# Kernel optimization log

Measured on AMD Instinct MI355X. Metric: run time of the kernel, lower is better.

Reference implementation:

```python
import jax, jax.numpy as jnp
import numpy as np

N = 100000
E = 3200000
CH_IN = 128
HID = 128
CH_OUT = 3


def setup_inputs() -> dict:
    key = jax.random.key(0)
    ks = jax.random.split(key, 16)
    def lin(kw, fan_in, fan_out):
        bound = 1.0 / np.sqrt(fan_in)
        kw1, kw2 = jax.random.split(kw)
        W = jax.random.uniform(kw1, (fan_in, fan_out), jnp.float32, -bound, bound)
        b = jax.random.uniform(kw2, (fan_out,), jnp.float32, -bound, bound)
        return W, b
    x = jax.random.normal(ks[0], (N, CH_IN), jnp.float32)
    edge_index = jax.random.randint(ks[1], (2, E), 0, N, jnp.int64)
    W1, b1 = lin(ks[2], CH_IN, HID)
    W2, b2 = lin(ks[3], HID, HID)
    lw1, lb1 = lin(ks[4], HID, HID)
    lw2, lb2 = lin(ks[5], HID, HID)
    lw3, lb3 = lin(ks[6], HID, HID)
    lw4, lb4 = lin(ks[7], HID, CH_OUT)
    return {"x": x, "edge_index": edge_index,
            "W1": W1, "b1": b1, "W2": W2, "b2": b2,
            "lw1": lw1, "lb1": lb1, "lw2": lw2, "lb2": lb2,
            "lw3": lw3, "lb3": lb3, "lw4": lw4, "lb4": lb4}


def gcn_conv(x, W, b, src, dst, n_nodes):
    xw = x @ W  # [N, H]
    ew = jnp.ones(src.shape[0], x.dtype)
    deg = jax.ops.segment_sum(ew, dst, num_segments=n_nodes) + 2.0  # +2 from improved self-loop
    dinv = jnp.where(deg > 0, jax.lax.rsqrt(deg), 0.0)
    norm = dinv[src] * dinv[dst]  # [E]
    agg = jax.ops.segment_sum(xw[src] * norm[:, None], dst, num_segments=n_nodes)
    # self-loop contribution: weight 2 * dinv[i]^2 * xw[i]
    agg = agg + xw * (2.0 * dinv * dinv)[:, None]
    return agg + b


def reference(x, edge_index, W1, b1, W2, b2, lw1, lb1, lw2, lb2, lw3, lb3, lw4, lb4):
    src, dst = edge_index[0], edge_index[1]
    n = x.shape[0]
    h = jnp.tanh(gcn_conv(x, W1, b1, src, dst, n))
    h = jnp.tanh(gcn_conv(h, W2, b2, src, dst, n))
    # dropout in eval mode = identity
    h = jnp.tanh(h @ lw1 + lb1)
    h = jnp.tanh(h @ lw2 + lb2)
    h = jnp.tanh(h @ lw3 + lb3)
    return h @ lw4 + lb4
```

## Files before the change

### kernel.cpp

```cpp
#include <hip/hip_runtime.h>

typedef __attribute__((ext_vector_type(8))) short short8;
typedef __attribute__((ext_vector_type(4))) float floatx4;
typedef __attribute__((ext_vector_type(4))) unsigned int uintx4;
typedef unsigned int uint32;

__device__ inline float b2f(unsigned short u) {
    union { uint32 i; float f; } x; x.i = ((uint32)u) << 16; return x.f;
}
__device__ inline float bl(uint32 v) {
    union { uint32 i; float f; } x; x.i = v << 16; return x.f;
}
__device__ inline float bh(uint32 v) {
    union { uint32 i; float f; } x; x.i = v & 0xffff0000u; return x.f;
}
__device__ inline unsigned short f2b(float f) {
    union { float f; uint32 u; } x; x.f = f;
    uint32 r = x.u + 0x7fffu + ((x.u >> 16) & 1u);
    return (unsigned short)(r >> 16);
}
__device__ inline float fast_tanh(float x) {
    float ax = __builtin_fabsf(x);
    float t = __builtin_amdgcn_exp2f(-2.8853900817779268f * ax);
    float r = (1.0f - t) * __builtin_amdgcn_rcpf(1.0f + t);
    return __builtin_copysignf(r, x);
}


#define CHUNK 8192
#define MAXBK 512
#define CAP   8704
#define LSTR  136

__global__ __launch_bounds__(512, 2) void scatterb_k(const int* __restrict__ eidx,
                                                     uint32* __restrict__ bkt_cur,
                                                     uint32* __restrict__ packed, int E,
                                                     const float* __restrict__ w0,
                                                     const float* __restrict__ w1,
                                                     const float* __restrict__ w2,
                                                     const float* __restrict__ w3,
                                                     const float* __restrict__ w4,
                                                     unsigned short* __restrict__ Wt_hi,
                                                     unsigned short* __restrict__ Wt_lo) {
    __shared__ uint32 hist[MAXBK];
    __shared__ uint32 hsc[MAXBK];
    __shared__ uint32 gbase[MAXBK];
    __shared__ uint32 lcur[MAXBK];
    __shared__ uint32 wsum[8];
    __shared__ uint32 stage[CHUNK];
    __shared__ unsigned short stgb[CHUNK];
    int t = threadIdx.x;

    if (blockIdx.x < 20) {
        int u = blockIdx.x * 512 + t;
        int widx = u >> 11;
        int f8 = u & 2047;
        const float* W;
        switch (widx) {
            case 0: W = w0; break;
            case 1: W = w1; break;
            case 2: W = w2; break;
            case 3: W = w3; break;
            default: W = w4; break;
        }
        int ct = f8 >> 8, kc = (f8 >> 6) & 3, quad = (f8 >> 4) & 3, r = f8 & 15;
        int c = ct * 16 + r;
        int kbase = kc * 32 + quad * 8;
        short8 hi8, lo8;
#pragma unroll
        for (int j = 0; j < 8; ++j) {
            float w = W[(kbase + j) * 128 + c];
            unsigned short h = f2b(w);
            hi8[j] = (short)h;
            lo8[j] = (short)f2b(w - b2f(h));
        }
        *(short8*)(Wt_hi + widx * 16384 + f8 * 8) = hi8;
        *(short8*)(Wt_lo + widx * 16384 + f8 * 8) = lo8;
    }

    int cbase = blockIdx.x * CHUNK;
    int n = E - cbase; if (n > CHUNK) n = CHUNK;

    hist[t] = 0;
    __syncthreads();
    int dreg[CHUNK / 512];
    int nt = 0;
    for (int i = t; i < n; i += 512) {
        int d = eidx[E + cbase + i];
        dreg[nt++] = d;
        atomicAdd(&hist[d >> 8], 1u);
    }
    __syncthreads();
    uint32 v = hist[t];
    uint32 x = v;
    int lane = t & 63;
#pragma unroll
    for (int off = 1; off < 64; off <<= 1) {
        uint32 y = __shfl_up(x, off);
        if (lane >= off) x += y;
    }
    if (lane == 63) wsum[t >> 6] = x;
    __syncthreads();
    uint32 pre = 0;
#pragma unroll
    for (int w = 0; w < 8; ++w) pre += (w < (t >> 6)) ? wsum[w] : 0;
    uint32 excl = x + pre - v;
    hsc[t] = excl;
    lcur[t] = excl;
    if (v) gbase[t] = (uint32)t * CAP + atomicAdd(&bkt_cur[t], v);
    __syncthreads();
    nt = 0;
    for (int i = t; i < n; i += 512) {
        int s = eidx[cbase + i];
        int d = dreg[nt++];
        int b = d >> 8;
        uint32 pos = atomicAdd(&lcur[b], 1u);
        stage[pos] = ((uint32)s << 8) | (uint32)(d & 255);
        stgb[pos] = (unsigned short)b;
    }
    __syncthreads();
    for (int i = t; i < n; i += 512) {
        int b = stgb[i];
        packed[gbase[b] + (i - hsc[b])] = stage[i];
    }
}


__global__ __launch_bounds__(256) void buildb_gemm_k(
    const uint32* __restrict__ packed,
    const uint32* __restrict__ bkt_cur,
    int* __restrict__ rowp, int* __restrict__ rowe,
    float* __restrict__ dinv, int* __restrict__ csr, int N, int NBK,
    const float* __restrict__ x,
    const unsigned short* __restrict__ Wt_hi,
    const unsigned short* __restrict__ Wt_lo,
    unsigned short* __restrict__ z1out) {
    __shared__ uint32 cnt[256];
    __shared__ uint32 cur[256];
    __shared__ uint32 wsum4[4];
    int t = threadIdx.x;
    int b = blockIdx.x;

    if (b >= NBK) {
        int gb = b - NBK;
        if (gb == 0 && t < 64) ((uint32*)z1out)[(size_t)N * 64 + t] = 0;
        int wave = t >> 6, lane = t & 63;
        int quad = lane >> 4, r = lane & 15;
        int m32 = gb * 128 + wave * 32;
        short8 af[2][4];
        const float4* Af = (const float4*)x;
#pragma unroll
        for (int s = 0; s < 2; ++s) {
            int rowA = m32 + s * 16 + r;
            if (rowA >= N) rowA = N - 1;
#pragma unroll
            for (int kc = 0; kc < 4; ++kc) {
                float4 p0 = Af[((size_t)rowA * 128 + kc * 32 + quad * 8) >> 2];
                float4 p1 = Af[(((size_t)rowA * 128 + kc * 32 + quad * 8) >> 2) + 1];
                short8 a;
                a[0] = (short)f2b(p0.x); a[1] = (short)f2b(p0.y);
                a[2] = (short)f2b(p0.z); a[3] = (short)f2b(p0.w);
                a[4] = (short)f2b(p1.x); a[5] = (short)f2b(p1.y);
                a[6] = (short)f2b(p1.z); a[7] = (short)f2b(p1.w);
                af[s][kc] = a;
            }
        }
        const short8* WhF = (const short8*)Wt_hi + lane;
        const short8* WlF = (const short8*)Wt_lo + lane;
#pragma unroll
        for (int ct = 0; ct < 8; ++ct) {
            int n = ct * 16 + r;
            floatx4 a0 = {0.f, 0.f, 0.f, 0.f}, a1 = {0.f, 0.f, 0.f, 0.f};
#pragma unroll
            for (int kc = 0; kc < 4; ++kc) {
                short8 bh8 = WhF[(ct * 4 + kc) << 6];
                a0 = __builtin_amdgcn_mfma_f32_16x16x32_bf16(af[0][kc], bh8, a0, 0, 0, 0);
                a1 = __builtin_amdgcn_mfma_f32_16x16x32_bf16(af[1][kc], bh8, a1, 0, 0, 0);
                short8 bl8 = WlF[(ct * 4 + kc) << 6];
                a0 = __builtin_amdgcn_mfma_f32_16x16x32_bf16(af[0][kc], bl8, a0, 0, 0, 0);
                a1 = __builtin_amdgcn_mfma_f32_16x16x32_bf16(af[1][kc], bl8, a1, 0, 0, 0);
            }
#pragma unroll
            for (int reg = 0; reg < 4; ++reg) {
                int i0 = m32 + quad * 4 + reg;
                if (i0 < N) z1out[(size_t)i0 * 128 + n] = f2b(a0[reg]);
                int i1 = m32 + 16 + quad * 4 + reg;
                if (i1 < N) z1out[(size_t)i1 * 128 + n] = f2b(a1[reg]);
            }
        }
        return;
    }

    if (b == 0 && t == 0) dinv[N] = 0.f;
    uint32 base = (uint32)b * CAP;
    uint32 size = bkt_cur[b];
    int node0 = b << 8;

    cnt[t] = 0;
    __syncthreads();
    for (uint32 i = t; i < size; i += 256)
        atomicAdd(&cnt[packed[base + i] & 255u], 1u);
    __syncthreads();
    uint32 v = cnt[t];
    uint32 x2 = v;
    int lane = t & 63;
#pragma unroll
    for (int off = 1; off < 64; off <<= 1) {
        uint32 y = __shfl_up(x2, off);
        if (lane >= off) x2 += y;
    }
    if (lane == 63) wsum4[t >> 6] = x2;
    __syncthreads();
    uint32 pre = 0;
#pragma unroll
    for (int w = 0; w < 4; ++w) pre += (w < (t >> 6)) ? wsum4[w] : 0;
    uint32 loc = x2 + pre - v;
    cur[t] = loc;
    int node = node0 + t;
    if (node < N) {
        dinv[node] = rsqrtf((float)v + 2.0f);
        rowp[node] = (int)(base + loc);
        rowe[node] = (int)(base + loc + v);
    }
    __syncthreads();
    for (uint32 i = t; i < size; i += 256) {
        uint32 p = packed[base + i];
        uint32 pos = atomicAdd(&cur[p & 255u], 1u);
        csr[base + pos] = (int)(p >> 8);
    }
}


__global__ __launch_bounds__(256, 4) void gemm_z_k(
    const unsigned short* __restrict__ Asrc,
    const unsigned short* __restrict__ Wt_hi,
    const unsigned short* __restrict__ Wt_lo,
    unsigned short* __restrict__ out, int N) {
    int tid = threadIdx.x;
    if (blockIdx.x == 0 && tid < 64) {
        ((uint32*)out)[(size_t)N * 64 + tid] = 0;
    }
    int wave = tid >> 6, lane = tid & 63;
    int quad = lane >> 4, r = lane & 15;
    int m32 = blockIdx.x * 128 + wave * 32;

    short8 af[2][4];
    const short* Ap = (const short*)Asrc;
#pragma unroll
    for (int s = 0; s < 2; ++s) {
        int rowA = m32 + s * 16 + r;
        if (rowA >= N) rowA = N - 1;
#pragma unroll
        for (int kc = 0; kc < 4; ++kc)
            af[s][kc] = *(const short8*)(Ap + (size_t)rowA * 128 + kc * 32 + quad * 8);
    }

    const short8* WhF = (const short8*)Wt_hi + lane;
    const short8* WlF = (const short8*)Wt_lo + lane;

#pragma unroll
    for (int ct = 0; ct < 8; ++ct) {
        int n = ct * 16 + r;
        floatx4 a0 = {0.f, 0.f, 0.f, 0.f}, a1 = {0.f, 0.f, 0.f, 0.f};
#pragma unroll
        for (int kc = 0; kc < 4; ++kc) {
            short8 bh8 = WhF[(ct * 4 + kc) << 6];
            a0 = __builtin_amdgcn_mfma_f32_16x16x32_bf16(af[0][kc], bh8, a0, 0, 0, 0);
            a1 = __builtin_amdgcn_mfma_f32_16x16x32_bf16(af[1][kc], bh8, a1, 0, 0, 0);
            short8 bl8 = WlF[(ct * 4 + kc) << 6];
            a0 = __builtin_amdgcn_mfma_f32_16x16x32_bf16(af[0][kc], bl8, a0, 0, 0, 0);
            a1 = __builtin_amdgcn_mfma_f32_16x16x32_bf16(af[1][kc], bl8, a1, 0, 0, 0);
        }
#pragma unroll
        for (int reg = 0; reg < 4; ++reg) {
            int i0 = m32 + quad * 4 + reg;
            if (i0 < N) out[(size_t)i0 * 128 + n] = f2b(a0[reg]);
            int i1 = m32 + 16 + quad * 4 + reg;
            if (i1 < N) out[(size_t)i1 * 128 + n] = f2b(a1[reg]);
        }
    }
}


__global__ __launch_bounds__(256, 2) void mlp_fused_k(
    const unsigned short* __restrict__ H,
    const unsigned short* __restrict__ WH,
    const unsigned short* __restrict__ WL,
    const float* __restrict__ lb1, const float* __restrict__ lb2,
    const float* __restrict__ lb3,
    const float* __restrict__ W4, const float* __restrict__ b4,
    float* __restrict__ out, int N) {
    __shared__ __align__(16) unsigned short wbuf[16384];
    __shared__ __align__(16) unsigned short tile[4][32 * LSTR];
    __shared__ float w4s[384];
    int tid = threadIdx.x;
    if (tid < 192) { w4s[tid] = W4[tid]; w4s[tid + 192] = W4[tid + 192]; }

    int wave = tid >> 6, lane = tid & 63;
    int quad = lane >> 4, r = lane & 15;
    unsigned short* T = tile[wave];
    int m32 = blockIdx.x * 128 + wave * 32;

    short8 af[2][4];
    const short* Hp = (const short*)H;
#pragma unroll
    for (int s = 0; s < 2; ++s) {
        int rowA = m32 + s * 16 + r;
        if (rowA >= N) rowA = N - 1;
#pragma unroll
        for (int kc = 0; kc < 4; ++kc)
            af[s][kc] = *(const short8*)(Hp + (size_t)rowA * 128 + kc * 32 + quad * 8);
    }

    const float* biases[3] = {lb1, lb2, lb3};
#pragma unroll
    for (int L = 0; L < 3; ++L) {
        const float* bias = biases[L];
        float bvv[8];
#pragma unroll
        for (int ct = 0; ct < 8; ++ct) bvv[ct] = bias[ct * 16 + r];
#pragma unroll
        for (int hf = 0; hf < 2; ++hf) {
            __syncthreads();
            {
                const uintx4* sh = (const uintx4*)(WH + L * 16384 + hf * 8192);
                const uintx4* sl = (const uintx4*)(WL + L * 16384 + hf * 8192);
                uintx4* dh = (uintx4*)wbuf;
                uintx4* dl = (uintx4*)(wbuf + 8192);
#pragma unroll
                for (int it = 0; it < 4; ++it) dh[tid + it * 256] = sh[tid + it * 256];
#pragma unroll
                for (int it = 0; it < 4; ++it) dl[tid + it * 256] = sl[tid + it * 256];
            }
            __syncthreads();
            const short8* whF = (const short8*)wbuf + lane;
            const short8* wlF = (const short8*)(wbuf + 8192) + lane;
#pragma unroll
            for (int c2 = 0; c2 < 4; ++c2) {
                int ct = hf * 4 + c2;
                int n = ct * 16 + r;
                floatx4 a0 = {0.f, 0.f, 0.f, 0.f}, a1 = {0.f, 0.f, 0.f, 0.f};
#pragma unroll
                for (int kc = 0; kc < 4; ++kc) {
                    short8 bh8 = whF[(c2 * 4 + kc) << 6];
                    a0 = __builtin_amdgcn_mfma_f32_16x16x32_bf16(af[0][kc], bh8, a0, 0, 0, 0);
                    a1 = __builtin_amdgcn_mfma_f32_16x16x32_bf16(af[1][kc], bh8, a1, 0, 0, 0);
                    short8 bl8 = wlF[(c2 * 4 + kc) << 6];
                    a0 = __builtin_amdgcn_mfma_f32_16x16x32_bf16(af[0][kc], bl8, a0, 0, 0, 0);
                    a1 = __builtin_amdgcn_mfma_f32_16x16x32_bf16(af[1][kc], bl8, a1, 0, 0, 0);
                }
                float bv = bvv[ct];
#pragma unroll
                for (int reg = 0; reg < 4; ++reg) {
                    int lrow = quad * 4 + reg;
                    T[lrow * LSTR + n] = f2b(fast_tanh(a0[reg] + bv));
                    T[(lrow + 16) * LSTR + n] = f2b(fast_tanh(a1[reg] + bv));
                }
            }
        }
        if (L < 2) {
#pragma unroll
            for (int s = 0; s < 2; ++s)
#pragma unroll
                for (int kc = 0; kc < 4; ++kc)
                    af[s][kc] = *(const short8*)&T[(s * 16 + r) * LSTR + kc * 32 + quad * 8];
        }
    }

    int lrow = lane & 31;
    int halfc = lane >> 5;
    float a0 = 0.f, a1 = 0.f, a2 = 0.f;
#pragma unroll
    for (int c8 = 0; c8 < 8; ++c8) {
        int cbase = halfc * 64 + c8 * 8;
        short8 hv = *(const short8*)&T[lrow * LSTR + cbase];
#pragma unroll
        for (int j = 0; j < 8; ++j) {
            float xv = b2f((unsigned short)hv[j]);
            int ch = cbase + j;
            a0 = fmaf(xv, w4s[ch * 3 + 0], a0);
            a1 = fmaf(xv, w4s[ch * 3 + 1], a1);
            a2 = fmaf(xv, w4s[ch * 3 + 2], a2);
        }
    }
    a0 += __shfl_xor(a0, 32);
    a1 += __shfl_xor(a1, 32);
    a2 += __shfl_xor(a2, 32);
    if (halfc == 0) {
        int i = m32 + lrow;
        if (i < N) {
            out[(size_t)i * 3 + 0] = a0 + b4[0];
            out[(size_t)i * 3 + 1] = a1 + b4[1];
            out[(size_t)i * 3 + 2] = a2 + b4[2];
        }
    }
}


__global__ __launch_bounds__(256) void agg_full_k(
    const uint32* __restrict__ z, const int* __restrict__ rowp,
    const int* __restrict__ rowe, const int* __restrict__ csr,
    const float* __restrict__ dinv, const float* __restrict__ bias,
    uint32* __restrict__ out, int N) {
    int lane = threadIdx.x & 63;
    int i = blockIdx.x * 4 + (threadIdx.x >> 6);
    if (i >= N) return;
    int start = rowp[i], end = rowe[i];
    const uint32* zl = z + lane;
    float a0 = 0.f, a1 = 0.f;
    for (int e = start; e < end; e += 64) {
        int cnt = end - e;
        if (cnt > 64) cnt = 64;
        int s = (lane < cnt) ? csr[e + lane] : N;
        float dv = dinv[s];
        int mp = (cnt + 15) & ~15;
        for (int m = 0; m < mp; m += 16) {
            uint32 v[16];
            float dvp[16];
#pragma unroll
            for (int p = 0; p < 16; ++p) {
                int sj = __shfl(s, m + p);
                dvp[p] = __shfl(dv, m + p);
                v[p] = zl[(size_t)sj << 6];
            }
#pragma unroll
            for (int p = 0; p < 16; ++p) {
                a0 = fmaf(dvp[p], bl(v[p]), a0);
                a1 = fmaf(dvp[p], bh(v[p]), a1);
            }
        }
    }
    float di = dinv[i];
    uint32 vi = zl[(size_t)i << 6];
    float di2 = 2.f * di;
    a0 = fmaf(di2, bl(vi), a0);
    a1 = fmaf(di2, bh(vi), a1);
    float2 bv = ((const float2*)bias)[lane];
    float h0 = fast_tanh(fmaf(di, a0, bv.x));
    float h1 = fast_tanh(fmaf(di, a1, bv.y));
    out[((size_t)i << 6) + lane] = (uint32)f2b(h0) | ((uint32)f2b(h1) << 16);
}

extern "C" void kernel_launch(void* const* d_in, const int* in_sizes, int n_in,
                              void* d_out, int out_size, void* d_ws, size_t ws_size,
                              hipStream_t stream) {
    const float* x   = (const float*)d_in[0];
    const int* eidx  = (const int*)d_in[1];
    const float* W1  = (const float*)d_in[2];
    const float* b1  = (const float*)d_in[3];
    const float* W2  = (const float*)d_in[4];
    const float* b2  = (const float*)d_in[5];
    const float* lw1 = (const float*)d_in[6];
    const float* lb1 = (const float*)d_in[7];
    const float* lw2 = (const float*)d_in[8];
    const float* lb2 = (const float*)d_in[9];
    const float* lw3 = (const float*)d_in[10];
    const float* lb3 = (const float*)d_in[11];
    const float* lw4 = (const float*)d_in[12];
    const float* lb4 = (const float*)d_in[13];
    float* out = (float*)d_out;

    const int N = in_sizes[0] / 128;
    const int E = in_sizes[1] / 2;

    char* p = (char*)d_ws;
    auto alloc = [&](size_t bytes) -> void* {
        void* q = (void*)p;
        p += (bytes + 255) & ~(size_t)255;
        return q;
    };
    const int NBK = (N + 255) >> 8;
    float* dinv      = (float*)alloc((size_t)(N + 1) * 4);
    int* rowp        = (int*)alloc((size_t)N * 4);
    int* rowe        = (int*)alloc((size_t)N * 4);
    uint32* bkt_cur  = (uint32*)alloc(MAXBK * 4);
    int* csr         = (int*)alloc((size_t)NBK * CAP * 4);
    unsigned short* Wt_hi = (unsigned short*)alloc(5 * 16384 * 2);
    unsigned short* Wt_lo = (unsigned short*)alloc(5 * 16384 * 2);
    unsigned short* bufA  = (unsigned short*)alloc((size_t)(N + 1) * 128 * 2);
    unsigned short* bufB  = (unsigned short*)alloc((size_t)(N + 1) * 128 * 2);
    uint32* packed = (uint32*)bufB;

    const int MB4 = (N + 127) / 128;
    const int AB  = (N + 3) / 4;
    const int NCH = (E + CHUNK - 1) / CHUNK;

    hipMemsetAsync(bkt_cur, 0, MAXBK * 4, stream);
    scatterb_k<<<NCH, 512, 0, stream>>>(eidx, bkt_cur, packed, E,
                                        W1, W2, lw1, lw2, lw3, Wt_hi, Wt_lo);
    buildb_gemm_k<<<NBK + MB4, 256, 0, stream>>>(packed, bkt_cur, rowp, rowe, dinv,
                                                 csr, N, NBK, x,
                                                 Wt_hi + 0 * 16384, Wt_lo + 0 * 16384,
                                                 bufA);

    const unsigned short* WH = Wt_hi;
    const unsigned short* WL = Wt_lo;

    agg_full_k<<<AB, 256, 0, stream>>>((const uint32*)bufA, rowp, rowe, csr, dinv, b1,
                                       (uint32*)bufB, N);
    gemm_z_k<<<MB4, 256, 0, stream>>>(bufB, WH + 1 * 16384, WL + 1 * 16384, bufA, N);
    agg_full_k<<<AB, 256, 0, stream>>>((const uint32*)bufA, rowp, rowe, csr, dinv, b2,
                                       (uint32*)bufB, N);
    mlp_fused_k<<<MB4, 256, 0, stream>>>(bufB, WH + 2 * 16384, WL + 2 * 16384,
                                         lb1, lb2, lb3, lw4, lb4, out, N);
}
```

Measured before the change: 453.0 us.

## Use column-blocked feature layout for first GCN aggregation to improve gather locality

Layer-1 features are now stored in 8 column groups of 16 bf16 values, one group per node row, instead of full 256-byte rows. A new aggregation kernel assigns each block one column group and processes two nodes per wave, gathering 32-byte slices. The intent is a smaller working set per pass so gathers hit cache better. The layer-2 GEMM reads the blocked layout through a template flag. The cost is that every CSR row is read 8 times, across more blocks.

```diff
diff --git a/kernel.cpp b/kernel.cpp
--- a/kernel.cpp
+++ b/kernel.cpp
@@ -140,10 +140,12 @@
     __shared__ uint32 wsum4[4];
     int t = threadIdx.x;
     int b = blockIdx.x;
+    const size_t Np1 = (size_t)N + 1;
 
     if (b >= NBK) {
         int gb = b - NBK;
-        if (gb == 0 && t < 64) ((uint32*)z1out)[(size_t)N * 64 + t] = 0;
+        if (gb == 0 && t < 64)
+            ((uint32*)z1out)[((size_t)(t >> 3) * Np1 + N) * 8 + (t & 7)] = 0;
         int wave = t >> 6, lane = t & 63;
         int quad = lane >> 4, r = lane & 15;
         int m32 = gb * 128 + wave * 32;
@@ -180,12 +182,13 @@
                 a0 = __builtin_amdgcn_mfma_f32_16x16x32_bf16(af[0][kc], bl8, a0, 0, 0, 0);
                 a1 = __builtin_amdgcn_mfma_f32_16x16x32_bf16(af[1][kc], bl8, a1, 0, 0, 0);
             }
+            int gg = n >> 4, c = n & 15;
 #pragma unroll
             for (int reg = 0; reg < 4; ++reg) {
                 int i0 = m32 + quad * 4 + reg;
-                if (i0 < N) z1out[(size_t)i0 * 128 + n] = f2b(a0[reg]);
+                if (i0 < N) z1out[((size_t)gg * Np1 + i0) * 16 + c] = f2b(a0[reg]);
                 int i1 = m32 + 16 + quad * 4 + reg;
-                if (i1 < N) z1out[(size_t)i1 * 128 + n] = f2b(a1[reg]);
+                if (i1 < N) z1out[((size_t)gg * Np1 + i1) * 16 + c] = f2b(a1[reg]);
             }
         }
         return;
@@ -231,12 +234,14 @@
 }
 
 
+template <int ASRC>
 __global__ __launch_bounds__(256, 4) void gemm_z_k(
     const unsigned short* __restrict__ Asrc,
     const unsigned short* __restrict__ Wt_hi,
     const unsigned short* __restrict__ Wt_lo,
     unsigned short* __restrict__ out, int N) {
     int tid = threadIdx.x;
+    const size_t Np1 = (size_t)N + 1;
     if (blockIdx.x == 0 && tid < 64) {
         ((uint32*)out)[(size_t)N * 64 + tid] = 0;
     }
@@ -251,8 +256,14 @@
         int rowA = m32 + s * 16 + r;
         if (rowA >= N) rowA = N - 1;
 #pragma unroll
-        for (int kc = 0; kc < 4; ++kc)
-            af[s][kc] = *(const short8*)(Ap + (size_t)rowA * 128 + kc * 32 + quad * 8);
+        for (int kc = 0; kc < 4; ++kc) {
+            if (ASRC == 2) {
+                int gg = kc * 2 + (quad >> 1);
+                af[s][kc] = *(const short8*)(Ap + ((size_t)gg * Np1 + rowA) * 16 + (quad & 1) * 8);
+            } else {
+                af[s][kc] = *(const short8*)(Ap + (size_t)rowA * 128 + kc * 32 + quad * 8);
+            }
+        }
     }
 
     const short8* WhF = (const short8*)Wt_hi + lane;
@@ -441,6 +452,90 @@
     out[((size_t)i << 6) + lane] = (uint32)f2b(h0) | ((uint32)f2b(h1) << 16);
 }
 
+
+__global__ __launch_bounds__(256) void agg_blk2_k(
+    const uint32* __restrict__ z, const int* __restrict__ rowp,
+    const int* __restrict__ rowe, const int* __restrict__ csr,
+    const float* __restrict__ dinv, const float* __restrict__ bias,
+    uint32* __restrict__ out, int N) {
+    int tid = threadIdx.x;
+    int wave = tid >> 6, lane = tid & 63;
+    int sg = lane >> 3, j = lane & 7;
+    int g = blockIdx.x & 7;
+    int chunk = blockIdx.x >> 3;
+    const size_t Np1 = (size_t)N + 1;
+    const uint32* zg = z + (size_t)g * Np1 * 8;
+    float2 bv = ((const float2*)bias)[g * 8 + j];
+    int ibase = chunk * 32 + wave * 8;
+
+#pragma unroll 1
+    for (int k = 0; k < 8; k += 2) {
+        int iA = ibase + k;
+        if (iA >= N) break;
+        int iB = iA + 1;
+        bool hasB = iB < N;
+        int iBc = hasB ? iB : iA;
+        int eA = rowp[iA], endA = rowe[iA];
+        int eB = rowp[iBc], endB = rowe[iBc];
+        float a0A = 0.f, a1A = 0.f, a0B = 0.f, a1B = 0.f;
+        for (; eA < endA || eB < endB; eA += 64, eB += 64) {
+            int cntA = endA - eA; cntA = cntA < 0 ? 0 : (cntA > 64 ? 64 : cntA);
+            int cntB = endB - eB; cntB = cntB < 0 ? 0 : (cntB > 64 ? 64 : cntB);
+            int sA = (lane < cntA) ? __builtin_nontemporal_load(&csr[eA + lane]) : N;
+            int sB = (lane < cntB) ? __builtin_nontemporal_load(&csr[eB + lane]) : N;
+            float dA = __builtin_nontemporal_load(&dinv[sA]);
+            float dB = __builtin_nontemporal_load(&dinv[sB]);
+            int cmax = cntA > cntB ? cntA : cntB;
+            int mp = (cmax + 31) & ~31;
+            for (int m = 0; m < mp; m += 32) {
+                uint32 vA4[4], vB4[4];
+                float dA4[4], dB4[4];
+#pragma unroll
+                for (int p = 0; p < 4; ++p) {
+                    int sj = __shfl(sA, m + p * 8 + sg);
+                    dA4[p] = __shfl(dA, m + p * 8 + sg);
+                    vA4[p] = zg[(size_t)sj * 8 + j];
+                }
+#pragma unroll
+                for (int p = 0; p < 4; ++p) {
+                    int sj = __shfl(sB, m + p * 8 + sg);
+                    dB4[p] = __shfl(dB, m + p * 8 + sg);
+                    vB4[p] = zg[(size_t)sj * 8 + j];
+                }
+#pragma unroll
+                for (int p = 0; p < 4; ++p) {
+                    a0A = fmaf(dA4[p], bl(vA4[p]), a0A);
+                    a1A = fmaf(dA4[p], bh(vA4[p]), a1A);
+                    a0B = fmaf(dB4[p], bl(vB4[p]), a0B);
+                    a1B = fmaf(dB4[p], bh(vB4[p]), a1B);
+                }
+            }
+        }
+        a0A += __shfl_xor(a0A, 8);  a0A += __shfl_xor(a0A, 16); a0A += __shfl_xor(a0A, 32);
+        a1A += __shfl_xor(a1A, 8);  a1A += __shfl_xor(a1A, 16); a1A += __shfl_xor(a1A, 32);
+        a0B += __shfl_xor(a0B, 8);  a0B += __shfl_xor(a0B, 16); a0B += __shfl_xor(a0B, 32);
+        a1B += __shfl_xor(a1B, 8);  a1B += __shfl_xor(a1B, 16); a1B += __shfl_xor(a1B, 32);
+        uint32 viA = zg[(size_t)iA * 8 + j];
+        float diA = dinv[iA];
+        a0A = fmaf(2.f * diA, bl(viA), a0A);
+        a1A = fmaf(2.f * diA, bh(viA), a1A);
+        float h0A = fast_tanh(fmaf(diA, a0A, bv.x));
+        float h1A = fast_tanh(fmaf(diA, a1A, bv.y));
+        if (sg == 0)
+            out[((size_t)g * Np1 + iA) * 8 + j] = (uint32)f2b(h0A) | ((uint32)f2b(h1A) << 16);
+        if (hasB) {
+            uint32 viB = zg[(size_t)iB * 8 + j];
+            float diB = dinv[iB];
+            a0B = fmaf(2.f * diB, bl(viB), a0B);
+            a1B = fmaf(2.f * diB, bh(viB), a1B);
+            float h0B = fast_tanh(fmaf(diB, a0B, bv.x));
+            float h1B = fast_tanh(fmaf(diB, a1B, bv.y));
+            if (sg == 0)
+                out[((size_t)g * Np1 + iB) * 8 + j] = (uint32)f2b(h0B) | ((uint32)f2b(h1B) << 16);
+        }
+    }
+}
+
 extern "C" void kernel_launch(void* const* d_in, const int* in_sizes, int n_in,
                               void* d_out, int out_size, void* d_ws, size_t ws_size,
                               hipStream_t stream) {
@@ -483,6 +578,7 @@
 
     const int MB4 = (N + 127) / 128;
     const int AB  = (N + 3) / 4;
+    const int ABLK = ((N + 31) / 32) * 8;
     const int NCH = (E + CHUNK - 1) / CHUNK;
 
     hipMemsetAsync(bkt_cur, 0, MAXBK * 4, stream);
@@ -496,9 +592,9 @@
     const unsigned short* WH = Wt_hi;
     const unsigned short* WL = Wt_lo;
 
-    agg_full_k<<<AB, 256, 0, stream>>>((const uint32*)bufA, rowp, rowe, csr, dinv, b1,
-                                       (uint32*)bufB, N);
-    gemm_z_k<<<MB4, 256, 0, stream>>>(bufB, WH + 1 * 16384, WL + 1 * 16384, bufA, N);
+    agg_blk2_k<<<ABLK, 256, 0, stream>>>((const uint32*)bufA, rowp, rowe, csr, dinv, b1,
+                                         (uint32*)bufB, N);
+    gemm_z_k<2><<<MB4, 256, 0, stream>>>(bufB, WH + 1 * 16384, WL + 1 * 16384, bufA, N);
     agg_full_k<<<AB, 256, 0, stream>>>((const uint32*)bufA, rowp, rowe, csr, dinv, b2,
                                        (uint32*)bufB, N);
     mlp_fused_k<<<MB4, 256, 0, stream>>>(bufB, WH + 2 * 16384, WL + 2 * 16384,
```

Result: slower. 739.6 us (+63.3%).
